# Kernel tuning notes

Hardware: AMD Instinct MI355X
Metric: run time of the kernel (lower is better)

## Reference

```python
import jax, jax.numpy as jnp
import numpy as np
import math

NUM_HEADS = 8
DIM = 512
DH = DIM // NUM_HEADS  # 64


def _rotary(x):
    # x: (b, l, h, s, d) ; interleaved-pair rotary (lucidrains RotaryEmbedding default)
    d = x.shape[-1]
    s = x.shape[-2]
    inv_freq = 1.0 / (10000.0 ** (jnp.arange(0, d, 2, dtype=jnp.float32) / d))  # (d/2,)
    t = jnp.arange(s, dtype=jnp.float32)
    freqs = t[:, None] * inv_freq[None, :]                # (s, d/2)
    freqs = jnp.repeat(freqs, 2, axis=-1)                 # (s, d) interleaved duplication
    cos = jnp.cos(freqs).astype(x.dtype)
    sin = jnp.sin(freqs).astype(x.dtype)
    x1 = x[..., 0::2]
    x2 = x[..., 1::2]
    rot = jnp.stack([-x2, x1], axis=-1).reshape(x.shape)  # rotate_half on interleaved pairs
    return x * cos + rot * sin


def setup_inputs() -> dict:
    key = jax.random.key(0)
    ks = jax.random.split(key, 9)
    b, l, s = 2, 2, 2048
    std = 1.0 / math.sqrt(DIM)
    inp = {
        "x": jax.random.normal(ks[0], (b, l, s, DIM), dtype=jnp.float32),
        "Wq": jax.random.normal(ks[1], (DIM, DIM), dtype=jnp.float32) * std,
        "bq": jnp.zeros((DIM,), dtype=jnp.float32),
        "Wk": jax.random.normal(ks[2], (DIM, DIM), dtype=jnp.float32) * std,
        "bk": jnp.zeros((DIM,), dtype=jnp.float32),
        "Wv": jax.random.normal(ks[3], (DIM, DIM), dtype=jnp.float32) * std,
        "bv": jnp.zeros((DIM,), dtype=jnp.float32),
        "Wo": jax.random.normal(ks[4], (DIM, DIM), dtype=jnp.float32) * std,
        "bo": jnp.zeros((DIM,), dtype=jnp.float32),
    }
    return inp


def reference(x, Wq, bq, Wk, bk, Wv, bv, Wo, bo):
    b, l, s, _ = x.shape
    h, dh = NUM_HEADS, DH

    def proj(W, bias):
        y = jnp.einsum('blsd,ed->blse', x, W) + bias      # nn.Linear: x @ W.T + b
        return y.reshape(b, l, s, h, dh).transpose(0, 1, 3, 2, 4)  # b l h s d

    q_proj = proj(Wq, bq)
    k_proj = proj(Wk, bk)
    v_proj = proj(Wv, bv)

    # Faithful to the source's swapped tuple unpack: k_mat <- V projection, v_mat <- K projection
    q_mat = _rotary(q_proj)
    k_mat = _rotary(v_proj)
    v_mat = k_proj

    scale = 1.0 / math.sqrt(dh * h)  # sqrt(dim), as in source
    scores = jnp.einsum('blhqd,blhkd->blhqk', q_mat, k_mat) * scale

    causal = jnp.tril(jnp.ones((s, s), dtype=bool))
    scores = jnp.where(causal[None, None, None], scores, -jnp.inf)

    weights = jax.nn.softmax(scores, axis=-1)
    inter = jnp.einsum('blhqk,blhkd->blhqd', weights, v_mat)
    inter = inter.transpose(0, 1, 3, 2, 4).reshape(b, l, s, h * dh)  # b l s (h d)
    out = jnp.einsum('blse,de->blsd', inter, Wo) + bo
    return out
```

## Files before the change

### kernel.cpp

```cpp
#include <hip/hip_runtime.h>
#include <math.h>

#define BB 2
#define LL 2
#define SS 2048
#define DD 512
#define HH 8
#define DHH 64

typedef __attribute__((ext_vector_type(8))) short bf16x8;
typedef __attribute__((ext_vector_type(4))) float f32x4;

#define MFMA16(a, b, c) __builtin_amdgcn_mfma_f32_16x16x32_bf16((a), (b), (c), 0, 0, 0)

#if __has_builtin(__builtin_amdgcn_exp2f)
#define EXP2F(x) __builtin_amdgcn_exp2f(x)
#else
#define EXP2F(x) exp2f(x)
#endif

#define PIPELINE_SYNC() asm volatile("s_waitcnt vmcnt(0)\n\ts_barrier" ::: "memory")

__device__ __forceinline__ unsigned short f2bf(float f) {
    union { float f; unsigned u; } x; x.f = f;
    unsigned u = x.u;
    return (unsigned short)((u + 0x7fffu + ((u >> 16) & 1u)) >> 16);
}

__device__ __forceinline__ unsigned bcast(float f) {
    union { float f; unsigned u; } x; x.f = f;
    return x.u;
}

__device__ __forceinline__ ushort4 pack4(float a, float b, float c, float d) {
    unsigned u0 = bcast(a) + 0x8000u, u1 = bcast(b) + 0x8000u;
    unsigned u2 = bcast(c) + 0x8000u, u3 = bcast(d) + 0x8000u;
    union { uint2 v; ushort4 s; } r;
    r.v.x = __builtin_amdgcn_perm(u1, u0, 0x07060302u);
    r.v.y = __builtin_amdgcn_perm(u3, u2, 0x07060302u);
    return r.s;
}

__device__ __forceinline__ void gload16(const unsigned short* g, unsigned short* l) {
    __builtin_amdgcn_global_load_lds(
        (const __attribute__((address_space(1))) unsigned int*)g,
        (__attribute__((address_space(3))) unsigned int*)l, 16, 0, 0);
}

__global__ __launch_bounds__(256) void prep_kernel(
    const float* __restrict__ x,  const float* __restrict__ wq,
    const float* __restrict__ wk, const float* __restrict__ wv,
    const float* __restrict__ wo, unsigned short* __restrict__ dst,
    float* __restrict__ cos_t, float* __restrict__ sin_t)
{
    int i = blockIdx.x * 256 + threadIdx.x;
    if (i < 1310720) {
        const float* src;
        int local;
        if (i < 1048576)      { src = x;  local = i; }
        else if (i < 1114112) { src = wq; local = i - 1048576; }
        else if (i < 1179648) { src = wk; local = i - 1114112; }
        else if (i < 1245184) { src = wv; local = i - 1179648; }
        else                  { src = wo; local = i - 1245184; }
        float4 v = ((const float4*)src)[local];
        ushort4 o;
        o.x = f2bf(v.x); o.y = f2bf(v.y); o.z = f2bf(v.z); o.w = f2bf(v.w);
        *(ushort4*)&dst[(size_t)i * 4] = o;
    } else {
        int idx = i - 1310720;
        int s = idx >> 5;
        int f = idx & 31;
        double inv = pow(10000.0, -(double)(2 * f) / (double)DHH);
        double ang = (double)s * inv;
        cos_t[idx] = (float)cos(ang);
        sin_t[idx] = (float)sin(ang);
    }
}

__global__ __launch_bounds__(256) void qkv_mfma_kernel(
    const unsigned short* __restrict__ xb,
    const unsigned short* __restrict__ wqb,
    const unsigned short* __restrict__ wkb,
    const unsigned short* __restrict__ wvb,
    const float* __restrict__ bq, const float* __restrict__ bk,
    const float* __restrict__ bv,
    const float* __restrict__ cos_t, const float* __restrict__ sin_t,
    unsigned short* __restrict__ qm, unsigned short* __restrict__ km,
    unsigned short* __restrict__ vt)
{
    __shared__ __align__(16) unsigned short As[2][4096];
    __shared__ __align__(16) unsigned short Bs[2][4096];

    const int tid  = threadIdx.x;
    const int w    = tid >> 6;
    const int lane = tid & 63;
    const int c    = lane & 15;
    const int quad = lane >> 4;
    const int mw   = (w & 1) * 64;
    const int nw   = (w >> 1) * 64;

    const int bx    = blockIdx.x;
    const int mat   = bx >> 2;
    const int nloc0 = (bx & 3) * 128;
    const int row0  = blockIdx.y * 128;

    const unsigned short* wsel = (mat == 0) ? wqb : (mat == 1) ? wkb : wvb;
    const float* bsel          = (mat == 0) ? bq  : (mat == 1) ? bk  : bv;

    const unsigned short* aSrc = (mat == 1) ? (xb   + (size_t)row0  * DD)
                                            : (wsel + (size_t)nloc0 * DD);
    const unsigned short* bSrc = (mat == 1) ? (wsel + (size_t)nloc0 * DD)
                                            : (xb   + (size_t)row0  * DD);

    auto stage = [&](int k0, int bb) {
        #pragma unroll
        for (int it = 0; it < 2; ++it) {
            int L   = it * 256 + tid;
            int row = L >> 2;
            int k8  = (L & 3) * 8;
            gload16(aSrc + (size_t)row * DD + k0 + k8, &As[bb][L * 8]);
            gload16(bSrc + (size_t)row * DD + k0 + k8, &Bs[bb][L * 8]);
        }
    };

    f32x4 acc[4][4];
    #pragma unroll
    for (int i = 0; i < 4; ++i)
        #pragma unroll
        for (int j = 0; j < 4; ++j)
            #pragma unroll
            for (int r = 0; r < 4; ++r) acc[i][j][r] = 0.f;

    stage(0, 0);

    for (int k0 = 0; k0 < DD; k0 += 32) {
        const int bb = (k0 >> 5) & 1;
        PIPELINE_SYNC();
        if (k0 + 32 < DD) stage(k0 + 32, bb ^ 1);

        bf16x8 af[4], bfr[4];
        #pragma unroll
        for (int mt = 0; mt < 4; ++mt)
            af[mt] = *(const bf16x8*)&As[bb][(mw + mt * 16 + c) * 32 + quad * 8];
        #pragma unroll
        for (int nt = 0; nt < 4; ++nt)
            bfr[nt] = *(const bf16x8*)&Bs[bb][(nw + nt * 16 + c) * 32 + quad * 8];
        #pragma unroll
        for (int mt = 0; mt < 4; ++mt)
            #pragma unroll
            for (int nt = 0; nt < 4; ++nt)
                acc[mt][nt] = MFMA16(af[mt], bfr[nt], acc[mt][nt]);
    }

    if (mat == 1) {
        #pragma unroll
        for (int nt = 0; nt < 4; ++nt) {
            int col = nloc0 + nw + nt * 16 + c;
            int h = col >> 6, dh = col & 63;
            float bias = bsel[col];
            #pragma unroll
            for (int mt = 0; mt < 4; ++mt) {
                int xr0 = row0 + mw + mt * 16 + quad * 4;
                int bl = xr0 >> 11, s0 = xr0 & 2047;
                ushort4 o = pack4(acc[mt][nt][0] + bias, acc[mt][nt][1] + bias,
                                  acc[mt][nt][2] + bias, acc[mt][nt][3] + bias);
                *(ushort4*)&vt[((size_t)(bl * HH + h) * DHH + dh) * SS + s0] = o;
            }
        }
    } else {
        unsigned short* dst = (mat == 0) ? qm : km;
        const float qscale = (mat == 0) ? 0.06375871448932861f : 1.0f;
        #pragma unroll
        for (int mt = 0; mt < 4; ++mt) {
            int col0 = nloc0 + mw + mt * 16 + quad * 4;
            int h = col0 >> 6, dh0 = col0 & 63;
            int f0 = dh0 >> 1;
            float4 bias4 = *(const float4*)&bsel[col0];
            #pragma unroll
            for (int nt = 0; nt < 4; ++nt) {
                int xr = row0 + nw + nt * 16 + c;
                int bl = xr >> 11, s = xr & 2047;
                float2 cs = *(const float2*)&cos_t[s * 32 + f0];
                float2 sn = *(const float2*)&sin_t[s * 32 + f0];
                float c0 = cs.x * qscale, s0v = sn.x * qscale;
                float c1 = cs.y * qscale, s1v = sn.y * qscale;
                float v0 = acc[mt][nt][0] + bias4.x;
                float v1 = acc[mt][nt][1] + bias4.y;
                float v2 = acc[mt][nt][2] + bias4.z;
                float v3 = acc[mt][nt][3] + bias4.w;
                ushort4 o = pack4(v0 * c0 - v1 * s0v, v1 * c0 + v0 * s0v,
                                  v2 * c1 - v3 * s1v, v3 * c1 + v2 * s1v);
                *(ushort4*)&dst[((size_t)(bl * HH + h) * SS + s) * DHH + dh0] = o;
            }
        }
    }
}

#define S_P 72

__global__ __launch_bounds__(256, 2) void attn_mfma_kernel(
    const unsigned short* __restrict__ qm,
    const unsigned short* __restrict__ km,
    const unsigned short* __restrict__ vt,
    unsigned short* __restrict__ inter)
{
    __shared__ __align__(16) unsigned short Ks[2][4096];
    __shared__ __align__(16) unsigned short Vs[2][4096];
    __shared__ __align__(16) unsigned short Ps[128 * S_P];

    const int tid  = threadIdx.x;
    const int w    = tid >> 6;
    const int lane = tid & 63;
    const int c    = lane & 15;
    const int quad = lane >> 4;

    const int h  = blockIdx.x;
    const int qt = 15 - blockIdx.y;
    const int bl = blockIdx.z;
    const int qw = qt * 128 + w * 32;

    const size_t seq_base = (size_t)(bl * HH + h) * SS * DHH;
    const size_t vt_base  = (size_t)(bl * HH + h) * DHH * SS;

    bf16x8 qf[2][2];
    #pragma unroll
    for (int nt = 0; nt < 2; ++nt)
        #pragma unroll
        for (int kk = 0; kk < 2; ++kk)
            qf[nt][kk] = *(const bf16x8*)(qm + seq_base +
                (size_t)(qw + nt * 16 + c) * DHH + kk * 32 + quad * 8);

    f32x4 oacc[4][2];
    f32x4 lacc[2];
    #pragma unroll
    for (int i = 0; i < 4; ++i)
        #pragma unroll
        for (int j = 0; j < 2; ++j)
            #pragma unroll
            for (int r = 0; r < 4; ++r) oacc[i][j][r] = 0.f;
    #pragma unroll
    for (int j = 0; j < 2; ++j)
        #pragma unroll
        for (int r = 0; r < 4; ++r) lacc[j][r] = 0.f;

    bf16x8 ones;
    #pragma unroll
    for (int i = 0; i < 8; ++i) ones[i] = (short)0x3F80;

    const int ntiles = 2 * qt + 2;

    auto stage = [&](int kt, int b) {
        const unsigned short* kg = km + seq_base + (size_t)(kt * 64) * DHH;
        const unsigned short* vg = vt + vt_base + kt * 64;
        #pragma unroll
        for (int it = 0; it < 2; ++it) {
            int L   = it * 256 + tid;
            int row = L >> 3;
            int gch = (L & 7) ^ (row & 7);
            gload16(kg + row * DHH + gch * 8, &Ks[b][L * 8]);
            gload16(vg + (size_t)row * SS + gch * 8, &Vs[b][L * 8]);
        }
    };

    stage(0, 0);

    for (int kt = 0; kt < ntiles; ++kt) {
        const int b = kt & 1;
        PIPELINE_SYNC();
        if (kt + 1 < ntiles) stage(kt + 1, b ^ 1);

        if (64 * kt <= qw + 31) {
            f32x4 sacc[4][2];
            #pragma unroll
            for (int mt = 0; mt < 4; ++mt)
                #pragma unroll
                for (int nt = 0; nt < 2; ++nt)
                    #pragma unroll
                    for (int r = 0; r < 4; ++r) sacc[mt][nt][r] = 0.f;
            #pragma unroll
            for (int kk = 0; kk < 2; ++kk) {
                bf16x8 kf[4];
                #pragma unroll
                for (int mt = 0; mt < 4; ++mt) {
                    int rr = mt * 16 + c;
                    kf[mt] = *(const bf16x8*)&Ks[b][rr * 64 +
                        (((kk * 4 + quad) ^ (rr & 7)) * 8)];
                }
                #pragma unroll
                for (int mt = 0; mt < 4; ++mt)
                    #pragma unroll
                    for (int nt = 0; nt < 2; ++nt)
                        sacc[mt][nt] = MFMA16(kf[mt], qf[nt][kk], sacc[mt][nt]);
            }

            const bool need_mask = (64 * kt + 63 > qw);
            #pragma unroll
            for (int mt = 0; mt < 4; ++mt) {
                #pragma unroll
                for (int nt = 0; nt < 2; ++nt) {
                    int q = qw + nt * 16 + c;
                    unsigned u[4];
                    #pragma unroll
                    for (int r = 0; r < 4; ++r) {
                        float p = EXP2F(sacc[mt][nt][r]);
                        if (need_mask) {
                            int key = kt * 64 + mt * 16 + quad * 4 + r;
                            if (key > q) p = 0.f;
                        }
                        u[r] = bcast(p) + 0x8000u;
                    }
                    uint2 d;
                    d.x = __builtin_amdgcn_perm(u[1], u[0], 0x07060302u);
                    d.y = __builtin_amdgcn_perm(u[3], u[2], 0x07060302u);
                    *(uint2*)&Ps[(w * 32 + nt * 16 + c) * S_P + mt * 16 + quad * 4] = d;
                }
            }

            #pragma unroll
            for (int kk = 0; kk < 2; ++kk) {
                bf16x8 bp[2];
                #pragma unroll
                for (int nt = 0; nt < 2; ++nt) {
                    bp[nt] = *(const bf16x8*)&Ps[(w * 32 + nt * 16 + c) * S_P +
                                                 kk * 32 + quad * 8];
                    lacc[nt] = MFMA16(ones, bp[nt], lacc[nt]);
                }
                #pragma unroll
                for (int mt4 = 0; mt4 < 4; ++mt4) {
                    int rv = mt4 * 16 + c;
                    bf16x8 av = *(const bf16x8*)&Vs[b][rv * 64 +
                        (((kk * 4 + quad) ^ (rv & 7)) * 8)];
                    oacc[mt4][0] = MFMA16(av, bp[0], oacc[mt4][0]);
                    oacc[mt4][1] = MFMA16(av, bp[1], oacc[mt4][1]);
                }
            }
        }
    }

    float invl0 = 1.f / lacc[0][0];
    float invl1 = 1.f / lacc[1][0];
    #pragma unroll
    for (int mt4 = 0; mt4 < 4; ++mt4) {
        int dh0 = mt4 * 16 + quad * 4;
        #pragma unroll
        for (int nt = 0; nt < 2; ++nt) {
            int query = qw + nt * 16 + c;
            float il = nt ? invl1 : invl0;
            ushort4 o;
            o.x = f2bf(oacc[mt4][nt][0] * il);
            o.y = f2bf(oacc[mt4][nt][1] * il);
            o.z = f2bf(oacc[mt4][nt][2] * il);
            o.w = f2bf(oacc[mt4][nt][3] * il);
            *(ushort4*)&inter[((size_t)bl * SS + query) * DD + h * DHH + dh0] = o;
        }
    }
}

__global__ __launch_bounds__(256) void outproj_mfma_kernel(
    const unsigned short* __restrict__ ib,
    const unsigned short* __restrict__ wob,
    const float* __restrict__ bo, float* __restrict__ out)
{
    __shared__ __align__(16) unsigned short As[2][2048];
    __shared__ __align__(16) unsigned short Bs[2][4096];

    const int tid  = threadIdx.x;
    const int w    = tid >> 6;
    const int lane = tid & 63;
    const int c    = lane & 15;
    const int quad = lane >> 4;
    const int mw   = (w & 1) * 32;
    const int nw   = (w >> 1) * 64;

    const int n0   = blockIdx.x * 64;
    const int row0 = blockIdx.y * 128;

    const unsigned short* aSrc = wob + (size_t)n0   * DD;
    const unsigned short* bSrc = ib  + (size_t)row0 * DD;

    auto stage = [&](int k0, int bb) {
        int L = tid;
        gload16(aSrc + (size_t)(L >> 2) * DD + k0 + (L & 3) * 8,
                &As[bb][L * 8]);
        #pragma unroll
        for (int it = 0; it < 2; ++it) {
            int L2 = it * 256 + tid;
            gload16(bSrc + (size_t)(L2 >> 2) * DD + k0 + (L2 & 3) * 8,
                    &Bs[bb][L2 * 8]);
        }
    };

    f32x4 acc[2][4];
    #pragma unroll
    for (int i = 0; i < 2; ++i)
        #pragma unroll
        for (int j = 0; j < 4; ++j)
            #pragma unroll
            for (int r = 0; r < 4; ++r) acc[i][j][r] = 0.f;

    stage(0, 0);

    for (int k0 = 0; k0 < DD; k0 += 32) {
        const int bb = (k0 >> 5) & 1;
        PIPELINE_SYNC();
        if (k0 + 32 < DD) stage(k0 + 32, bb ^ 1);

        bf16x8 af[2], bfr[4];
        #pragma unroll
        for (int mt = 0; mt < 2; ++mt)
            af[mt] = *(const bf16x8*)&As[bb][(mw + mt * 16 + c) * 32 + quad * 8];
        #pragma unroll
        for (int nt = 0; nt < 4; ++nt)
            bfr[nt] = *(const bf16x8*)&Bs[bb][(nw + nt * 16 + c) * 32 + quad * 8];
        #pragma unroll
        for (int mt = 0; mt < 2; ++mt)
            #pragma unroll
            for (int nt = 0; nt < 4; ++nt)
                acc[mt][nt] = MFMA16(af[mt], bfr[nt], acc[mt][nt]);
    }

    #pragma unroll
    for (int mt = 0; mt < 2; ++mt) {
        int col0 = n0 + mw + mt * 16 + quad * 4;
        float4 b4 = *(const float4*)&bo[col0];
        #pragma unroll
        for (int nt = 0; nt < 4; ++nt) {
            int xr = row0 + nw + nt * 16 + c;
            float4 o;
            o.x = acc[mt][nt][0] + b4.x;
            o.y = acc[mt][nt][1] + b4.y;
            o.z = acc[mt][nt][2] + b4.z;
            o.w = acc[mt][nt][3] + b4.w;
            *(float4*)&out[(size_t)xr * DD + col0] = o;
        }
    }
}

extern "C" void kernel_launch(void* const* d_in, const int* in_sizes, int n_in,
                              void* d_out, int out_size, void* d_ws, size_t ws_size,
                              hipStream_t stream)
{
    const float* x  = (const float*)d_in[0];
    const float* Wq = (const float*)d_in[1];
    const float* bq = (const float*)d_in[2];
    const float* Wk = (const float*)d_in[3];
    const float* bk = (const float*)d_in[4];
    const float* Wv = (const float*)d_in[5];
    const float* bv = (const float*)d_in[6];
    const float* Wo = (const float*)d_in[7];
    const float* bo = (const float*)d_in[8];
    float* out = (float*)d_out;
    char* ws = (char*)d_ws;

    unsigned short* inter = (unsigned short*)(ws);
    float* cos_t = (float*)(ws + 8388608);
    float* sin_t = (float*)(ws + 8650752);
    unsigned short* xb  = (unsigned short*)(ws + 8912896);
    unsigned short* wqb = (unsigned short*)(ws + 17301504);
    unsigned short* wkb = (unsigned short*)(ws + 17825792);
    unsigned short* wvb = (unsigned short*)(ws + 18350080);
    unsigned short* wob = (unsigned short*)(ws + 18874368);
    unsigned short* qm  = (unsigned short*)(ws + 19398656);
    unsigned short* km  = (unsigned short*)(ws + 27787264);
    unsigned short* vt  = (unsigned short*)(ws + 36175872);

    prep_kernel<<<dim3(5376), dim3(256), 0, stream>>>(
        x, Wq, Wk, Wv, Wo, xb, cos_t, sin_t);
    qkv_mfma_kernel<<<dim3(12, 64), dim3(256), 0, stream>>>(
        xb, wqb, wkb, wvb, bq, bk, bv, cos_t, sin_t, qm, km, vt);
    attn_mfma_kernel<<<dim3(HH, 16, BB * LL), dim3(256), 0, stream>>>(qm, km, vt, inter);
    outproj_mfma_kernel<<<dim3(8, 64), dim3(256), 0, stream>>>(inter, wob, bo, out);
}
```

Measured before the change: 194.6 us.

## Pair causal query tiles per block and stage attention output via LDS

The attention kernel moves from 128-query tiles (one per block, heavy tiles first) to 64-query tiles. Each block processes a complementary pair (qt and 31-qt), so every block does the same total amount of causal work. Each wave now handles 16 queries instead of 32, and the output is staged through shared memory for coalesced 16-byte global stores. This aims to fix load imbalance and tail effects. In exchange, key/value tiles are reloaded for each 64-row query tile, which doubles K/V traffic per query and halves MFMA reuse per K/V load.

```diff
diff --git a/kernel.cpp b/kernel.cpp
--- a/kernel.cpp
+++ b/kernel.cpp
@@ -206,7 +206,7 @@
 {
     __shared__ __align__(16) unsigned short Ks[2][4096];
     __shared__ __align__(16) unsigned short Vs[2][4096];
-    __shared__ __align__(16) unsigned short Ps[128 * S_P];
+    __shared__ __align__(16) unsigned short Ps[64 * S_P];
 
     const int tid  = threadIdx.x;
     const int w    = tid >> 6;
@@ -214,40 +214,17 @@
     const int c    = lane & 15;
     const int quad = lane >> 4;
 
-    const int h  = blockIdx.x;
-    const int qt = 15 - blockIdx.y;
-    const int bl = blockIdx.z;
-    const int qw = qt * 128 + w * 32;
-
-    const size_t seq_base = (size_t)(bl * HH + h) * SS * DHH;
-    const size_t vt_base  = (size_t)(bl * HH + h) * DHH * SS;
-
-    bf16x8 qf[2][2];
-    #pragma unroll
-    for (int nt = 0; nt < 2; ++nt)
-        #pragma unroll
-        for (int kk = 0; kk < 2; ++kk)
-            qf[nt][kk] = *(const bf16x8*)(qm + seq_base +
-                (size_t)(qw + nt * 16 + c) * DHH + kk * 32 + quad * 8);
-
-    f32x4 oacc[4][2];
-    f32x4 lacc[2];
-    #pragma unroll
-    for (int i = 0; i < 4; ++i)
-        #pragma unroll
-        for (int j = 0; j < 2; ++j)
-            #pragma unroll
-            for (int r = 0; r < 4; ++r) oacc[i][j][r] = 0.f;
-    #pragma unroll
-    for (int j = 0; j < 2; ++j)
-        #pragma unroll
-        for (int r = 0; r < 4; ++r) lacc[j][r] = 0.f;
+    const int pair = blockIdx.x;
+    const int blh  = blockIdx.y;
+    const int h    = blh & 7;
+    const int bl   = blh >> 3;
+
+    const size_t seq_base = (size_t)blh * SS * DHH;
+    const size_t vt_base  = (size_t)blh * DHH * SS;
 
     bf16x8 ones;
     #pragma unroll
     for (int i = 0; i < 8; ++i) ones[i] = (short)0x3F80;
-
-    const int ntiles = 2 * qt + 2;
 
     auto stage = [&](int kt, int b) {
         const unsigned short* kg = km + seq_base + (size_t)(kt * 64) * DHH;
@@ -262,21 +239,38 @@
         }
     };
 
-    stage(0, 0);
-
-    for (int kt = 0; kt < ntiles; ++kt) {
-        const int b = kt & 1;
-        PIPELINE_SYNC();
-        if (kt + 1 < ntiles) stage(kt + 1, b ^ 1);
-
-        if (64 * kt <= qw + 31) {
-            f32x4 sacc[4][2];
+    for (int leg = 0; leg < 2; ++leg) {
+        const int qt     = leg ? pair : (31 - pair);
+        const int ntiles = qt + 1;
+        const int qw     = qt * 64 + w * 16;
+
+        bf16x8 qf[2];
+        #pragma unroll
+        for (int kk = 0; kk < 2; ++kk)
+            qf[kk] = *(const bf16x8*)(qm + seq_base +
+                (size_t)(qw + c) * DHH + kk * 32 + quad * 8);
+
+        f32x4 oacc[4];
+        f32x4 lacc;
+        #pragma unroll
+        for (int i = 0; i < 4; ++i)
+            #pragma unroll
+            for (int r = 0; r < 4; ++r) oacc[i][r] = 0.f;
+        #pragma unroll
+        for (int r = 0; r < 4; ++r) lacc[r] = 0.f;
+
+        stage(0, 0);
+
+        for (int kt = 0; kt < ntiles; ++kt) {
+            const int b = kt & 1;
+            PIPELINE_SYNC();
+            if (kt + 1 < ntiles) stage(kt + 1, b ^ 1);
+
+            f32x4 sacc[4];
             #pragma unroll
             for (int mt = 0; mt < 4; ++mt)
                 #pragma unroll
-                for (int nt = 0; nt < 2; ++nt)
-                    #pragma unroll
-                    for (int r = 0; r < 4; ++r) sacc[mt][nt][r] = 0.f;
+                for (int r = 0; r < 4; ++r) sacc[mt][r] = 0.f;
             #pragma unroll
             for (int kk = 0; kk < 2; ++kk) {
                 bf16x8 kf[4];
@@ -288,71 +282,62 @@
                 }
                 #pragma unroll
                 for (int mt = 0; mt < 4; ++mt)
-                    #pragma unroll
-                    for (int nt = 0; nt < 2; ++nt)
-                        sacc[mt][nt] = MFMA16(kf[mt], qf[nt][kk], sacc[mt][nt]);
+                    sacc[mt] = MFMA16(kf[mt], qf[kk], sacc[mt]);
             }
 
-            const bool need_mask = (64 * kt + 63 > qw);
+            const bool need_mask = (kt == qt);
+            const int q = qw + c;
             #pragma unroll
             for (int mt = 0; mt < 4; ++mt) {
+                unsigned u[4];
                 #pragma unroll
-                for (int nt = 0; nt < 2; ++nt) {
-                    int q = qw + nt * 16 + c;
-                    unsigned u[4];
-                    #pragma unroll
-                    for (int r = 0; r < 4; ++r) {
-                        float p = EXP2F(sacc[mt][nt][r]);
-                        if (need_mask) {
-                            int key = kt * 64 + mt * 16 + quad * 4 + r;
-                            if (key > q) p = 0.f;
-                        }
-                        u[r] = bcast(p) + 0x8000u;
+                for (int r = 0; r < 4; ++r) {
+                    float p = EXP2F(sacc[mt][r]);
+                    if (need_mask) {
+                        int key = kt * 64 + mt * 16 + quad * 4 + r;
+                        if (key > q) p = 0.f;
                     }
-                    uint2 d;
-                    d.x = __builtin_amdgcn_perm(u[1], u[0], 0x07060302u);
-                    d.y = __builtin_amdgcn_perm(u[3], u[2], 0x07060302u);
-                    *(uint2*)&Ps[(w * 32 + nt * 16 + c) * S_P + mt * 16 + quad * 4] = d;
+                    u[r] = bcast(p) + 0x8000u;
                 }
+                uint2 d;
+                d.x = __builtin_amdgcn_perm(u[1], u[0], 0x07060302u);
+                d.y = __builtin_amdgcn_perm(u[3], u[2], 0x07060302u);
+                *(uint2*)&Ps[(w * 16 + c) * S_P + mt * 16 + quad * 4] = d;
             }
 
             #pragma unroll
             for (int kk = 0; kk < 2; ++kk) {
-                bf16x8 bp[2];
-                #pragma unroll
-                for (int nt = 0; nt < 2; ++nt) {
-                    bp[nt] = *(const bf16x8*)&Ps[(w * 32 + nt * 16 + c) * S_P +
-                                                 kk * 32 + quad * 8];
-                    lacc[nt] = MFMA16(ones, bp[nt], lacc[nt]);
-                }
+                bf16x8 bp = *(const bf16x8*)&Ps[(w * 16 + c) * S_P +
+                                                kk * 32 + quad * 8];
+                lacc = MFMA16(ones, bp, lacc);
                 #pragma unroll
                 for (int mt4 = 0; mt4 < 4; ++mt4) {
                     int rv = mt4 * 16 + c;
                     bf16x8 av = *(const bf16x8*)&Vs[b][rv * 64 +
                         (((kk * 4 + quad) ^ (rv & 7)) * 8)];
-                    oacc[mt4][0] = MFMA16(av, bp[0], oacc[mt4][0]);
-                    oacc[mt4][1] = MFMA16(av, bp[1], oacc[mt4][1]);
+                    oacc[mt4] = MFMA16(av, bp, oacc[mt4]);
                 }
             }
         }
-    }
-
-    float invl0 = 1.f / lacc[0][0];
-    float invl1 = 1.f / lacc[1][0];
-    #pragma unroll
-    for (int mt4 = 0; mt4 < 4; ++mt4) {
-        int dh0 = mt4 * 16 + quad * 4;
-        #pragma unroll
-        for (int nt = 0; nt < 2; ++nt) {
-            int query = qw + nt * 16 + c;
-            float il = nt ? invl1 : invl0;
-            ushort4 o;
-            o.x = f2bf(oacc[mt4][nt][0] * il);
-            o.y = f2bf(oacc[mt4][nt][1] * il);
-            o.z = f2bf(oacc[mt4][nt][2] * il);
-            o.w = f2bf(oacc[mt4][nt][3] * il);
-            *(ushort4*)&inter[((size_t)bl * SS + query) * DD + h * DHH + dh0] = o;
-        }
+
+        float il = 1.f / lacc[0];
+        #pragma unroll
+        for (int mt4 = 0; mt4 < 4; ++mt4) {
+            ushort4 o = pack4(oacc[mt4][0] * il, oacc[mt4][1] * il,
+                              oacc[mt4][2] * il, oacc[mt4][3] * il);
+            *(ushort4*)&Ps[(w * 16 + c) * S_P + mt4 * 16 + quad * 4] = o;
+        }
+        __syncthreads();
+        #pragma unroll
+        for (int pass = 0; pass < 2; ++pass) {
+            int idx  = pass * 256 + tid;
+            int srow = idx >> 3;
+            int chnk = idx & 7;
+            bf16x8 v = *(const bf16x8*)&Ps[srow * S_P + chnk * 8];
+            *(bf16x8*)&inter[((size_t)bl * SS + qt * 64 + srow) * DD +
+                             h * DHH + chnk * 8] = v;
+        }
+        __syncthreads();
     }
 }
 
@@ -468,6 +453,6 @@
         x, Wq, Wk, Wv, Wo, xb, cos_t, sin_t);
     qkv_mfma_kernel<<<dim3(12, 64), dim3(256), 0, stream>>>(
         xb, wqb, wkb, wvb, bq, bk, bv, cos_t, sin_t, qm, km, vt);
-    attn_mfma_kernel<<<dim3(HH, 16, BB * LL), dim3(256), 0, stream>>>(qm, km, vt, inter);
+    attn_mfma_kernel<<<dim3(16, 32), dim3(256), 0, stream>>>(qm, km, vt, inter);
     outproj_mfma_kernel<<<dim3(8, 64), dim3(256), 0, stream>>>(inter, wob, bo, out);
 }
```

Result: faster. 177.9 us (-8.6%).
